# Kernel tuning notes

Measured on AMD Instinct MI355X. Metric: run time of the kernel, lower is better.

## Reference

```python
import jax, jax.numpy as jnp
import numpy as np

LEAKY_SLOPE = 0.2  # nn.LeakyReLU(alpha) with alpha=0.2
NEG_MASK = -9e15   # matches -9000000000000000.0 in the torch source


def _leaky_relu(x):
    return jnp.where(x > 0, x, LEAKY_SLOPE * x)


def setup_inputs() -> dict:
    key = jax.random.key(0)
    kh, ka, k0, k1, k2, k3 = jax.random.split(key, 6)
    B, N, D = 512, 256, 128
    hidden = jax.random.normal(kh, (B, N, D), dtype=jnp.float32)
    adj = jax.random.randint(ka, (B, N, N), 0, 5, dtype=jnp.int32)
    a_0 = jax.random.normal(k0, (D, 1), dtype=jnp.float32) * 0.05
    a_1 = jax.random.normal(k1, (D, 1), dtype=jnp.float32) * 0.05
    a_2 = jax.random.normal(k2, (D, 1), dtype=jnp.float32) * 0.05
    a_3 = jax.random.normal(k3, (D, 1), dtype=jnp.float32) * 0.05
    return {"hidden": hidden, "adj": adj, "a_0": a_0, "a_1": a_1, "a_2": a_2, "a_3": a_3}


def reference(hidden, adj, a_0, a_1, a_2, a_3):
    # hidden: [B, N, D]; adj: [B, N, N] int with relation ids in {0..4}
    # Original builds a_input[b,i,j,:] = hidden[b,i,:] * hidden[b,j,:] then
    # e_r = leakyrelu(a_input @ a_r). Equivalent (same math, no N*N*D blowup):
    # e_r[b,i,j] = leakyrelu( sum_d hidden[b,i,d] * a_r[d] * hidden[b,j,d] ).
    h = hidden

    def rel_scores(a_r):
        hw = h * a_r[:, 0][None, None, :]           # [B, N, D]
        return _leaky_relu(jnp.einsum('bid,bjd->bij', hw, h))  # [B, N, N]

    e_0 = rel_scores(a_0)
    e_1 = rel_scores(a_1)
    e_2 = rel_scores(a_2)
    e_3 = rel_scores(a_3)

    scores = jnp.full_like(e_0, NEG_MASK)
    scores = jnp.where(adj == 1, e_0, scores)
    scores = jnp.where(adj == 2, e_1, scores)
    scores = jnp.where(adj == 3, e_2, scores)
    scores = jnp.where(adj == 4, e_3, scores)

    alpha = jax.nn.softmax(scores, axis=-1)         # [B, N, N]
    return jnp.einsum('bij,bjd->bid', alpha, h)     # [B, N, D]
```

## Files before the change

### kernel.cpp

```cpp
#include <hip/hip_runtime.h>
#include <hip/hip_bf16.h>

typedef short bf16x8 __attribute__((ext_vector_type(8)));
typedef float f32x4  __attribute__((ext_vector_type(4)));
typedef __fp16 fp16x2 __attribute__((ext_vector_type(2)));

#define NB 512
#define NN 256
#define ND 128
#define H_STRIDE 136
#define HT_STRIDE 264
#define SMEM_SHORTS (NN*H_STRIDE + ND*HT_STRIDE + 4*ND)
#define SMEM_BYTES (SMEM_SHORTS * 2)

__device__ __forceinline__ short f2b(float f) {
    __hip_bfloat16 h = __float2bfloat16(f);
    union { __hip_bfloat16 b; short s; } u; u.b = h;
    return u.s;
}
__device__ __forceinline__ float b2f(short s) {
    union { unsigned u; float f; } v; v.u = ((unsigned)(unsigned short)s) << 16;
    return v.f;
}
__device__ __forceinline__ unsigned pack_f16(float a, float b) {
    union { fp16x2 v; unsigned u; } x;
    x.v = __builtin_amdgcn_cvt_pkrtz(a, b);
    return x.u;
}
__device__ __forceinline__ float unp_lo(unsigned u) {
    union { unsigned short s; __fp16 h; } x; x.s = (unsigned short)(u & 0xffffu);
    return (float)x.h;
}
__device__ __forceinline__ float unp_hi(unsigned u) {
    union { unsigned short s; __fp16 h; } x; x.s = (unsigned short)(u >> 16);
    return (float)x.h;
}

__global__ __attribute__((amdgpu_flat_work_group_size(512, 512)))
__attribute__((amdgpu_waves_per_eu(2, 2)))
void gat_fused(const float* __restrict__ hidden, const int* __restrict__ adj,
               const float* __restrict__ a0, const float* __restrict__ a1,
               const float* __restrict__ a2, const float* __restrict__ a3,
               float* __restrict__ out)
{
    extern __shared__ short smem[];
    short* s_h  = smem;
    short* s_ht = s_h + NN * H_STRIDE;
    short* s_a  = s_ht + ND * HT_STRIDE;

    const int b    = blockIdx.x;
    const int tid  = threadIdx.x;
    const int wave = tid >> 6;
    const int lane = tid & 63;
    const int c = lane & 15;
    const int g = lane >> 4;

    int srcl[4];
    #pragma unroll
    for (int r = 0; r < 4; ++r) srcl[r] = c + 16 * (((8 * g + 2 * r) & 15) >> 2);

    const float* hb = hidden + (size_t)b * (NN * ND);
    for (int idx = tid * 4; idx < NN * ND; idx += 512 * 4) {
        const float4 v = *(const float4*)(hb + idx);
        const int j = idx >> 7, d = idx & (ND - 1);
        union { short s[4]; uint2 u; } pkv;
        pkv.s[0] = f2b(v.x); pkv.s[1] = f2b(v.y); pkv.s[2] = f2b(v.z); pkv.s[3] = f2b(v.w);
        *(uint2*)&s_h[j * H_STRIDE + d] = pkv.u;
    }
    {
        const float* ap = (tid < 128) ? a0 : (tid < 256) ? a1 : (tid < 384) ? a2 : a3;
        s_a[tid] = f2b(ap[tid & 127]);
    }
    __syncthreads();

    #pragma unroll
    for (int iter = 0; iter < 8; ++iter) {
        const int task = wave + 8 * iter;
        const int d0 = (task & 15) * 8;
        const int j0 = (task >> 4) * 64;
        union { short s[8]; uint4 u; } pkv;
        pkv.u = *(const uint4*)&s_h[(j0 + lane) * H_STRIDE + d0];
        #pragma unroll
        for (int e = 0; e < 8; ++e)
            s_ht[(d0 + e) * HT_STRIDE + j0 + lane] = pkv.s[e];
    }
    __syncthreads();

    const int* adj_b = adj + ((size_t)b << 16);
    float* out_b = out + (size_t)b * (NN * ND);

    for (int n = 0; n < 2; ++n) {
        const int it = wave + 8 * n;
        const int ibase = it * 16;

        unsigned avpk4[8];
        #pragma unroll
        for (int jt2 = 0; jt2 < 8; ++jt2) {
            const int4 aA = *(const int4*)&adj_b[(ibase + c) * NN + (2 * jt2) * 16 + 4 * g];
            const int4 aB = *(const int4*)&adj_b[(ibase + c) * NN + (2 * jt2 + 1) * 16 + 4 * g];
            avpk4[jt2] = (unsigned)aA.x | ((unsigned)aA.y << 4) |
                         ((unsigned)aA.z << 8) | ((unsigned)aA.w << 12) |
                         ((unsigned)aB.x << 16) | ((unsigned)aB.y << 20) |
                         ((unsigned)aB.z << 24) | ((unsigned)aB.w << 28);
        }
        __builtin_amdgcn_sched_barrier(0);

        unsigned scp[16][2];
        float m = -3.0e38f;

        {
            bf16x8 qs[2][4];
            #pragma unroll
            for (int s = 0; s < 4; ++s) {
                const bf16x8 q = *(const bf16x8*)&s_h[(ibase + c) * H_STRIDE + s * 32 + g * 8];
                #pragma unroll
                for (int r = 0; r < 2; ++r) {
                    const bf16x8 av = *(const bf16x8*)&s_a[r * ND + s * 32 + g * 8];
                    bf16x8 o;
                    #pragma unroll
                    for (int e = 0; e < 8; ++e) o[e] = f2b(b2f(q[e]) * b2f(av[e]));
                    qs[r][s] = o;
                }
            }
            #pragma unroll
            for (int jt = 0; jt < 16; ++jt) {
                if ((jt & 1) == 0) __builtin_amdgcn_sched_barrier(0);
                const int jbase = jt * 16;
                f32x4 e0 = {0.f,0.f,0.f,0.f}, e1 = {0.f,0.f,0.f,0.f};
                #pragma unroll
                for (int s = 0; s < 4; ++s) {
                    const bf16x8 hj = *(const bf16x8*)&s_h[(jbase + c) * H_STRIDE + s * 32 + g * 8];
                    e0 = __builtin_amdgcn_mfma_f32_16x16x32_bf16(hj, qs[0][s], e0, 0, 0, 0);
                    e1 = __builtin_amdgcn_mfma_f32_16x16x32_bf16(hj, qs[1][s], e1, 0, 0, 0);
                }
                const unsigned apk = avpk4[jt >> 1] >> ((jt & 1) * 16);
                float v[4];
                #pragma unroll
                for (int q = 0; q < 4; ++q) {
                    const int a = (apk >> (4 * q)) & 0xf;
                    v[q] = (a == 1) ? e0[q] : (a == 2) ? e1[q] : -9.0e15f;
                }
                scp[jt][0] = pack_f16(v[0], v[1]);
                scp[jt][1] = pack_f16(v[2], v[3]);
            }
        }

        {
            bf16x8 qs[2][4];
            #pragma unroll
            for (int s = 0; s < 4; ++s) {
                const bf16x8 q = *(const bf16x8*)&s_h[(ibase + c) * H_STRIDE + s * 32 + g * 8];
                #pragma unroll
                for (int r = 0; r < 2; ++r) {
                    const bf16x8 av = *(const bf16x8*)&s_a[(r + 2) * ND + s * 32 + g * 8];
                    bf16x8 o;
                    #pragma unroll
                    for (int e = 0; e < 8; ++e) o[e] = f2b(b2f(q[e]) * b2f(av[e]));
                    qs[r][s] = o;
                }
            }
            #pragma unroll
            for (int jt = 0; jt < 16; ++jt) {
                if ((jt & 1) == 0) __builtin_amdgcn_sched_barrier(0);
                const int jbase = jt * 16;
                f32x4 e2 = {0.f,0.f,0.f,0.f}, e3 = {0.f,0.f,0.f,0.f};
                #pragma unroll
                for (int s = 0; s < 4; ++s) {
                    const bf16x8 hj = *(const bf16x8*)&s_h[(jbase + c) * H_STRIDE + s * 32 + g * 8];
                    e2 = __builtin_amdgcn_mfma_f32_16x16x32_bf16(hj, qs[0][s], e2, 0, 0, 0);
                    e3 = __builtin_amdgcn_mfma_f32_16x16x32_bf16(hj, qs[1][s], e3, 0, 0, 0);
                }
                const unsigned apk = avpk4[jt >> 1] >> ((jt & 1) * 16);
                float v[4];
                #pragma unroll
                for (int q = 0; q < 4; ++q) {
                    const int a = (apk >> (4 * q)) & 0xf;
                    const float prev = (q == 0) ? unp_lo(scp[jt][0]) :
                                       (q == 1) ? unp_hi(scp[jt][0]) :
                                       (q == 2) ? unp_lo(scp[jt][1]) : unp_hi(scp[jt][1]);
                    float e = (a == 3) ? e2[q] : (a == 4) ? e3[q] : prev;
                    e = e > 0.f ? e : 0.2f * e;
                    m = fmaxf(m, e);
                    v[q] = e;
                }
                scp[jt][0] = pack_f16(v[0], v[1]);
                scp[jt][1] = pack_f16(v[2], v[3]);
            }
        }

        m = fmaxf(m, __shfl_xor(m, 16));
        m = fmaxf(m, __shfl_xor(m, 32));
        float sum = 0.f;
        #pragma unroll
        for (int jt = 0; jt < 16; ++jt) {
            const float p0 = __expf(unp_lo(scp[jt][0]) - m);
            const float p1 = __expf(unp_hi(scp[jt][0]) - m);
            const float p2 = __expf(unp_lo(scp[jt][1]) - m);
            const float p3 = __expf(unp_hi(scp[jt][1]) - m);
            sum += (p0 + p1) + (p2 + p3);
            scp[jt][0] = ((unsigned)(unsigned short)f2b(p0)) |
                         (((unsigned)(unsigned short)f2b(p1)) << 16);
            scp[jt][1] = ((unsigned)(unsigned short)f2b(p2)) |
                         (((unsigned)(unsigned short)f2b(p3)) << 16);
        }
        sum += __shfl_xor(sum, 16);
        sum += __shfl_xor(sum, 32);
        const float rinv = 1.f / sum;
        float rq[4];
        #pragma unroll
        for (int q = 0; q < 4; ++q) rq[q] = __shfl(rinv, 4 * g + q, 64);

        f32x4 oacc[8];
        #pragma unroll
        for (int dt = 0; dt < 8; ++dt) oacc[dt] = (f32x4){0.f,0.f,0.f,0.f};
        #pragma unroll
        for (int ph = 0; ph < 8; ++ph) {
            union { unsigned u[4]; bf16x8 v; } pa;
            #pragma unroll
            for (int r = 0; r < 4; ++r) {
                const unsigned lo = __shfl(scp[2 * ph][r & 1], srcl[r], 64);
                const unsigned hi = __shfl(scp[2 * ph + 1][r & 1], srcl[r], 64);
                pa.u[r] = (g >= 2) ? hi : lo;
            }
            #pragma unroll
            for (int dt = 0; dt < 8; ++dt) {
                const bf16x8 vb = *(const bf16x8*)
                    &s_ht[(dt * 16 + c) * HT_STRIDE + ph * 32 + g * 8];
                oacc[dt] = __builtin_amdgcn_mfma_f32_16x16x32_bf16(pa.v, vb, oacc[dt], 0, 0, 0);
            }
        }

        #pragma unroll
        for (int dt = 0; dt < 8; ++dt)
            #pragma unroll
            for (int q = 0; q < 4; ++q)
                out_b[(ibase + 4 * g + q) * ND + dt * 16 + c] = oacc[dt][q] * rq[q];
    }
}

extern "C" void kernel_launch(void* const* d_in, const int* in_sizes, int n_in,
                              void* d_out, int out_size, void* d_ws, size_t ws_size,
                              hipStream_t stream) {
    const float* hidden = (const float*)d_in[0];
    const int*   adjp   = (const int*)d_in[1];
    const float* a0 = (const float*)d_in[2];
    const float* a1 = (const float*)d_in[3];
    const float* a2 = (const float*)d_in[4];
    const float* a3 = (const float*)d_in[5];
    float* outp = (float*)d_out;

    (void)hipFuncSetAttribute((const void*)gat_fused,
                              hipFuncAttributeMaxDynamicSharedMemorySize, SMEM_BYTES);
    gat_fused<<<dim3(NB), dim3(512), SMEM_BYTES, stream>>>(hidden, adjp, a0, a1, a2, a3, outp);
}
```

Baseline: 87.35 us.

## Fuse four relation score passes into one loop and raise MFMA wave priority

Merges the two score passes, each computing two relations, into a single pass that computes all four relation MFMAs per j-tile. Each h_j tile is then read from LDS once instead of twice, and the fp16 pack/unpack of intermediate scores goes away. Scores are clamped to -60000 so the masked value stays finite in fp16. s_setprio is raised around the MFMA blocks so MFMA-issuing waves get priority. Holding four sets of scaled query fragments in registers raises VGPR pressure, which may reduce occupancy.

```diff
diff --git a/kernel.cpp b/kernel.cpp
--- a/kernel.cpp
+++ b/kernel.cpp
@@ -108,84 +108,50 @@
         unsigned scp[16][2];
         float m = -3.0e38f;
 
-        {
-            bf16x8 qs[2][4];
+        bf16x8 qs[4][4];
+        #pragma unroll
+        for (int s = 0; s < 4; ++s) {
+            const bf16x8 q = *(const bf16x8*)&s_h[(ibase + c) * H_STRIDE + s * 32 + g * 8];
+            #pragma unroll
+            for (int r = 0; r < 4; ++r) {
+                const bf16x8 av = *(const bf16x8*)&s_a[r * ND + s * 32 + g * 8];
+                bf16x8 o;
+                #pragma unroll
+                for (int e = 0; e < 8; ++e) o[e] = f2b(b2f(q[e]) * b2f(av[e]));
+                qs[r][s] = o;
+            }
+        }
+
+        #pragma unroll
+        for (int jt = 0; jt < 16; ++jt) {
+            __builtin_amdgcn_sched_barrier(0);
+            const int jbase = jt * 16;
+            f32x4 e0 = {0.f,0.f,0.f,0.f}, e1 = {0.f,0.f,0.f,0.f};
+            f32x4 e2 = {0.f,0.f,0.f,0.f}, e3 = {0.f,0.f,0.f,0.f};
+            __builtin_amdgcn_s_setprio(1);
             #pragma unroll
             for (int s = 0; s < 4; ++s) {
-                const bf16x8 q = *(const bf16x8*)&s_h[(ibase + c) * H_STRIDE + s * 32 + g * 8];
-                #pragma unroll
-                for (int r = 0; r < 2; ++r) {
-                    const bf16x8 av = *(const bf16x8*)&s_a[r * ND + s * 32 + g * 8];
-                    bf16x8 o;
-                    #pragma unroll
-                    for (int e = 0; e < 8; ++e) o[e] = f2b(b2f(q[e]) * b2f(av[e]));
-                    qs[r][s] = o;
-                }
-            }
-            #pragma unroll
-            for (int jt = 0; jt < 16; ++jt) {
-                if ((jt & 1) == 0) __builtin_amdgcn_sched_barrier(0);
-                const int jbase = jt * 16;
-                f32x4 e0 = {0.f,0.f,0.f,0.f}, e1 = {0.f,0.f,0.f,0.f};
-                #pragma unroll
-                for (int s = 0; s < 4; ++s) {
-                    const bf16x8 hj = *(const bf16x8*)&s_h[(jbase + c) * H_STRIDE + s * 32 + g * 8];
-                    e0 = __builtin_amdgcn_mfma_f32_16x16x32_bf16(hj, qs[0][s], e0, 0, 0, 0);
-                    e1 = __builtin_amdgcn_mfma_f32_16x16x32_bf16(hj, qs[1][s], e1, 0, 0, 0);
-                }
-                const unsigned apk = avpk4[jt >> 1] >> ((jt & 1) * 16);
-                float v[4];
-                #pragma unroll
-                for (int q = 0; q < 4; ++q) {
-                    const int a = (apk >> (4 * q)) & 0xf;
-                    v[q] = (a == 1) ? e0[q] : (a == 2) ? e1[q] : -9.0e15f;
-                }
-                scp[jt][0] = pack_f16(v[0], v[1]);
-                scp[jt][1] = pack_f16(v[2], v[3]);
-            }
-        }
-
-        {
-            bf16x8 qs[2][4];
-            #pragma unroll
-            for (int s = 0; s < 4; ++s) {
-                const bf16x8 q = *(const bf16x8*)&s_h[(ibase + c) * H_STRIDE + s * 32 + g * 8];
-                #pragma unroll
-                for (int r = 0; r < 2; ++r) {
-                    const bf16x8 av = *(const bf16x8*)&s_a[(r + 2) * ND + s * 32 + g * 8];
-                    bf16x8 o;
-                    #pragma unroll
-                    for (int e = 0; e < 8; ++e) o[e] = f2b(b2f(q[e]) * b2f(av[e]));
-                    qs[r][s] = o;
-                }
-            }
-            #pragma unroll
-            for (int jt = 0; jt < 16; ++jt) {
-                if ((jt & 1) == 0) __builtin_amdgcn_sched_barrier(0);
-                const int jbase = jt * 16;
-                f32x4 e2 = {0.f,0.f,0.f,0.f}, e3 = {0.f,0.f,0.f,0.f};
-                #pragma unroll
-                for (int s = 0; s < 4; ++s) {
-                    const bf16x8 hj = *(const bf16x8*)&s_h[(jbase + c) * H_STRIDE + s * 32 + g * 8];
-                    e2 = __builtin_amdgcn_mfma_f32_16x16x32_bf16(hj, qs[0][s], e2, 0, 0, 0);
-                    e3 = __builtin_amdgcn_mfma_f32_16x16x32_bf16(hj, qs[1][s], e3, 0, 0, 0);
-                }
-                const unsigned apk = avpk4[jt >> 1] >> ((jt & 1) * 16);
-                float v[4];
-                #pragma unroll
-                for (int q = 0; q < 4; ++q) {
-                    const int a = (apk >> (4 * q)) & 0xf;
-                    const float prev = (q == 0) ? unp_lo(scp[jt][0]) :
-                                       (q == 1) ? unp_hi(scp[jt][0]) :
-                                       (q == 2) ? unp_lo(scp[jt][1]) : unp_hi(scp[jt][1]);
-                    float e = (a == 3) ? e2[q] : (a == 4) ? e3[q] : prev;
-                    e = e > 0.f ? e : 0.2f * e;
-                    m = fmaxf(m, e);
-                    v[q] = e;
-                }
-                scp[jt][0] = pack_f16(v[0], v[1]);
-                scp[jt][1] = pack_f16(v[2], v[3]);
-            }
+                const bf16x8 hj = *(const bf16x8*)&s_h[(jbase + c) * H_STRIDE + s * 32 + g * 8];
+                e0 = __builtin_amdgcn_mfma_f32_16x16x32_bf16(hj, qs[0][s], e0, 0, 0, 0);
+                e1 = __builtin_amdgcn_mfma_f32_16x16x32_bf16(hj, qs[1][s], e1, 0, 0, 0);
+                e2 = __builtin_amdgcn_mfma_f32_16x16x32_bf16(hj, qs[2][s], e2, 0, 0, 0);
+                e3 = __builtin_amdgcn_mfma_f32_16x16x32_bf16(hj, qs[3][s], e3, 0, 0, 0);
+            }
+            __builtin_amdgcn_s_setprio(0);
+            const unsigned apk = avpk4[jt >> 1] >> ((jt & 1) * 16);
+            float v[4];
+            #pragma unroll
+            for (int q = 0; q < 4; ++q) {
+                const int a = (apk >> (4 * q)) & 0xf;
+                float e = (a == 1) ? e0[q] : (a == 2) ? e1[q] :
+                          (a == 3) ? e2[q] : (a == 4) ? e3[q] : -9.0e15f;
+                e = e > 0.f ? e : 0.2f * e;
+                e = fmaxf(e, -60000.f);
+                m = fmaxf(m, e);
+                v[q] = e;
+            }
+            scp[jt][0] = pack_f16(v[0], v[1]);
+            scp[jt][1] = pack_f16(v[2], v[3]);
         }
 
         m = fmaxf(m, __shfl_xor(m, 16));
@@ -222,12 +188,14 @@
                 const unsigned hi = __shfl(scp[2 * ph + 1][r & 1], srcl[r], 64);
                 pa.u[r] = (g >= 2) ? hi : lo;
             }
+            __builtin_amdgcn_s_setprio(1);
             #pragma unroll
             for (int dt = 0; dt < 8; ++dt) {
                 const bf16x8 vb = *(const bf16x8*)
                     &s_ht[(dt * 16 + c) * HT_STRIDE + ph * 32 + g * 8];
                 oacc[dt] = __builtin_amdgcn_mfma_f32_16x16x32_bf16(pa.v, vb, oacc[dt], 0, 0, 0);
             }
+            __builtin_amdgcn_s_setprio(0);
         }
 
         #pragma unroll
```

Result: slower. 100.6 us (+15.2%).
